# Performance work log

Hardware: AMD Instinct MI355X
Metric: run time of the kernel (lower is better)

The kernel has to match this reference:

```python
import jax, jax.numpy as jnp
import numpy as np
import math

B, L, D, H = 4, 1024, 768, 12   # docs, seq_len, hidden, attn heads
E, M, P = 24, 4, 552            # entities/doc, mentions/entity, pairs/doc
EMB, BLK, NL = 768, 64, 97      # emb_size, block_size, num relation labels


def setup_inputs() -> dict:
    key = jax.random.key(0)
    ks = jax.random.split(key, 12)
    s = 0.02  # weight init scale
    return {
        "sequence_output": jax.random.normal(ks[0], (B, L, D), jnp.float32),
        "attention": jax.random.uniform(ks[1], (B, H, L, L), jnp.float32),
        "W_q": jax.random.normal(ks[2], (D, D), jnp.float32) * s,
        "W_k": jax.random.normal(ks[3], (D, D), jnp.float32) * s,
        "head_W": jax.random.normal(ks[4], (2 * D, EMB), jnp.float32) * s,
        "head_b": jax.random.normal(ks[5], (EMB,), jnp.float32) * s,
        "tail_W": jax.random.normal(ks[6], (2 * D, EMB), jnp.float32) * s,
        "tail_b": jax.random.normal(ks[7], (EMB,), jnp.float32) * s,
        "bil_W": jax.random.normal(ks[8], (EMB * BLK, NL), jnp.float32) * s,
        "bil_b": jax.random.normal(ks[9], (NL,), jnp.float32) * s,
        "mention_pos": jax.random.randint(ks[10], (B, E, M), 0, L - 2),
        "hts": jax.random.randint(ks[11], (B, P, 2), 0, E),
    }


def reference(sequence_output, attention, W_q, W_k, head_W, head_b,
              tail_W, tail_b, bil_W, bil_b, mention_pos, hts):
    offset = 1  # bert-style [CLS] offset
    pos = mention_pos + offset                     # [B,E,M] token index of each mention
    bb = jnp.arange(B)[:, None, None]

    # --- mention gathers (padded version of the ragged python loops) ---
    # per-mention attention rows: attention[b, :, pos, :] -> [B,E,M,H,L]
    att_q = attention.transpose(0, 2, 1, 3)        # [B,L,H,L]
    ment_att = att_q[bb, pos]                      # [B,E,M,H,L]
    ent_att = ment_att.mean(axis=2)                # [B,E,H,L]  (mean over mentions)
    # mention embeddings (GAT stage = identity here): [B,E,M,D]
    ment_emb = sequence_output[bb, pos]

    # --- localized context rs via head*tail attention product ---
    bb2 = jnp.arange(B)[:, None]
    h_att = ent_att[bb2, hts[:, :, 0]]             # [B,P,H,L]
    t_att = ent_att[bb2, hts[:, :, 1]]             # [B,P,H,L]
    ht_att = (h_att * t_att).mean(axis=2)          # [B,P,L] (mean over heads)
    ht_att = ht_att / (ht_att.sum(axis=-1, keepdims=True) + 1e-5)
    rs = jnp.einsum('bld,bpl->bpd', sequence_output, ht_att)  # [B,P,D]

    R = B * P
    rs_f = rs.reshape(R, D)

    # --- entity representations via mention-level attention pooling ---
    h_ment = ment_emb[bb2, hts[:, :, 0]].reshape(R, M, D)
    t_ment = ment_emb[bb2, hts[:, :, 1]].reshape(R, M, D)
    q_c = rs_f @ W_q                               # [R,D]
    inv = 1.0 / math.sqrt(D)

    def pool(ment):
        k = ment.reshape(-1, D) @ W_k
        k = k.reshape(R, M, D)
        scores = jnp.einsum('rmd,rd->rm', k, q_c) * inv
        w = jax.nn.softmax(scores, axis=-1)
        return jnp.einsum('rm,rmd->rd', w, ment)

    h_ent = pool(h_ment)                           # [R,D]
    t_ent = pool(t_ment)                           # [R,D]

    # --- extractors + grouped bilinear classifier ---
    hs = jnp.tanh(jnp.concatenate([h_ent, rs_f], axis=1) @ head_W + head_b)
    ts = jnp.tanh(jnp.concatenate([t_ent, rs_f], axis=1) @ tail_W + tail_b)
    K = EMB // BLK
    b1 = hs.reshape(R, K, BLK)
    b2 = ts.reshape(R, K, BLK)
    bl = (b1[:, :, :, None] * b2[:, :, None, :]).reshape(R, EMB * BLK)
    logits = bl @ bil_W + bil_b                    # [R,NL]
    return logits
```

## Files before the change

### kernel.cpp

```cpp
#include <hip/hip_runtime.h>
#include <hip/hip_bf16.h>
#include <math.h>

#define Bc 4
#define Lc 1024
#define Dc 768
#define Hc 12
#define Ec 24
#define Mc 4
#define Pc 552
#define EMBc 768
#define NLc 97
#define Rc (Bc*Pc)
#define KSPL 48
#define HT_ABS (35*32*512)

typedef __attribute__((ext_vector_type(4))) float f32x4;
typedef __attribute__((ext_vector_type(8))) short short8;
typedef __attribute__((ext_vector_type(4))) unsigned short us4;
typedef _Float16 f16x8 __attribute__((ext_vector_type(8)));

static __device__ __forceinline__ unsigned short f2bf(float x){
  unsigned int u = __float_as_uint(x);
  unsigned int r = u + 0x7fffu + ((u >> 16) & 1u);
  return (unsigned short)(r >> 16);
}
static __device__ __forceinline__ unsigned short f2h(float x){
  _Float16 h = (_Float16)x;
  return __builtin_bit_cast(unsigned short, h);
}
static __device__ __forceinline__ float h2f(unsigned short x){
  return (float)__builtin_bit_cast(_Float16, x);
}
static __device__ __forceinline__ size_t flin_off(int r, int kk, int KT){
  return ((size_t)(r>>4)*KT + (kk>>5))*512 + (size_t)((((kk&31)>>3)*16 + (r&15))*8) + (kk&7);
}

__global__ __launch_bounds__(256) void k_prep(const float* __restrict__ bilW, unsigned short* __restrict__ Wbf,
                                              const float* __restrict__ seq, unsigned short* __restrict__ seqf,
                                              const float* __restrict__ W_q, unsigned short* __restrict__ Wq_f,
                                              const float* __restrict__ W_k, unsigned short* __restrict__ Wk_f,
                                              const float* __restrict__ headW, unsigned short* __restrict__ headW_f,
                                              const float* __restrict__ tailW, unsigned short* __restrict__ tailW_f,
                                              const float* __restrict__ att, const int* __restrict__ mpos,
                                              float* __restrict__ ent_att,
                                              unsigned short* __restrict__ ment_bf){
  int bx = blockIdx.x;
  int tid = threadIdx.x;
  __shared__ float t[64][65];
  if (bx < 1536){
    const float* Ws = bilW + (size_t)bx*32*NLc;
    unsigned short* o = Wbf + (size_t)bx*4480;
    float* w = &t[0][0];
    for (int idx = tid; idx < 32*NLc; idx += 256)
      w[idx] = Ws[idx];
    __syncthreads();
    #pragma unroll
    for (int q8 = 0; q8 < 18; q8++){
      int idx = q8*256 + tid;
      if (idx < 4480){
        int n = idx / 40, kk = idx - n*40;
        float v = (kk < 32 && n < NLc) ? w[kk*NLc + n] : 0.f;
        o[idx] = f2h(v);
      }
    }
    return;
  }
  if (bx >= 3168){
    int blk = bx - 3168;
    int h  = blk % Hc;
    int be = blk / Hc;
    int b  = be / Ec;
    int p0 = mpos[be*Mc+0]+1, p1 = mpos[be*Mc+1]+1;
    int p2 = mpos[be*Mc+2]+1, p3 = mpos[be*Mc+3]+1;
    const float* ab = att + ((size_t)b*Hc + h)*Lc*Lc;
    const float* a0 = ab + (size_t)p0*Lc;
    const float* a1 = ab + (size_t)p1*Lc;
    const float* a2 = ab + (size_t)p2*Lc;
    const float* a3 = ab + (size_t)p3*Lc;
    float* o = ent_att + (size_t)blk*Lc;
    int l4 = tid*4;
    float4 v0 = *(const float4*)(a0 + l4);
    float4 v1 = *(const float4*)(a1 + l4);
    float4 v2 = *(const float4*)(a2 + l4);
    float4 v3 = *(const float4*)(a3 + l4);
    float4 ov;
    ov.x = 0.25f*(v0.x+v1.x+v2.x+v3.x);
    ov.y = 0.25f*(v0.y+v1.y+v2.y+v3.y);
    ov.z = 0.25f*(v0.z+v1.z+v2.z+v3.z);
    ov.w = 0.25f*(v0.w+v1.w+v2.w+v3.w);
    *(float4*)(o + l4) = ov;
    int gidx = blk*256 + tid;
    int d = gidx % Dc;
    int bem = gidx / Dc;
    int bb = bem / (Ec*Mc);
    int pos = mpos[bem] + 1;
    float v = seq[((size_t)bb*Lc + pos)*Dc + d];
    ment_bf[flin_off(bem, d, 24)] = f2bf(v);
    return;
  }
  bx -= 1536;
  const float* src; unsigned short* dst; int tk, tn, KTW;
  if (bx < 768){
    int z = bx / 192, rem = bx % 192;
    src = seq + (size_t)z*Lc*Dc; dst = seqf + (size_t)z*(Dc/16)*(Lc/32)*512;
    tk = rem % 16; tn = rem / 16; KTW = 32;
  } else if (bx < 768+144){
    int rem = bx - 768;
    src = W_q; dst = Wq_f; tk = rem % 12; tn = rem / 12; KTW = 24;
  } else if (bx < 768+288){
    int rem = bx - (768+144);
    src = W_k; dst = Wk_f; tk = rem % 12; tn = rem / 12; KTW = 24;
  } else if (bx < 768+288+288){
    int rem = bx - (768+288);
    src = headW; dst = headW_f; tk = rem % 24; tn = rem / 24; KTW = 48;
  } else {
    int rem = bx - (768+288+288);
    src = tailW; dst = tailW_f; tk = rem % 24; tn = rem / 24; KTW = 48;
  }
  int r0 = tk*64, c0 = tn*64;
  #pragma unroll
  for (int q8 = 0; q8 < 16; q8++){
    int idx = q8*256 + tid;
    int rr = idx >> 6, cc = idx & 63;
    t[rr][cc] = src[(size_t)(r0+rr)*768 + c0+cc];
  }
  __syncthreads();
  #pragma unroll
  for (int q8 = 0; q8 < 16; q8++){
    int idx = q8*256 + tid;
    int li = idx & 511, sub = idx >> 9;
    int nt_l = sub >> 1, kt_l = sub & 1;
    int lane = li >> 3, e = li & 7;
    int kl = kt_l*32 + (lane>>4)*8 + e;
    int nl = nt_l*16 + (lane&15);
    dst[ ((size_t)(c0/16 + nt_l)*KTW + (r0/32 + kt_l))*512 + li ] = f2bf(t[kl][nl]);
  }
}

__global__ __launch_bounds__(256) void k_ht_att(const float* __restrict__ ent_att,
                                                const int* __restrict__ hts,
                                                unsigned short* __restrict__ htbf){
  int b = blockIdx.x & 3;
  int p = blockIdx.x >> 2;
  unsigned short* o = htbf + (size_t)b*HT_ABS;
  int l4 = threadIdx.x*4;
  if (p >= Pc){
    us4 z4 = {0,0,0,0};
    *(us4*)(o + flin_off(p, l4, 32)) = z4;
    return;
  }
  int r = b*Pc + p;
  int hi = hts[r*2+0], ti = hts[r*2+1];
  const float* eh = ent_att + (size_t)(b*Ec+hi)*Hc*Lc;
  const float* et = ent_att + (size_t)(b*Ec+ti)*Hc*Lc;
  __shared__ float raw[Lc];
  __shared__ float wsum[4];
  float4 s4 = {0.f,0.f,0.f,0.f};
  #pragma unroll
  for (int h = 0; h < Hc; h++){
    float4 e1 = *(const float4*)&eh[h*Lc + l4];
    float4 e2 = *(const float4*)&et[h*Lc + l4];
    s4.x = fmaf(e1.x,e2.x,s4.x); s4.y = fmaf(e1.y,e2.y,s4.y);
    s4.z = fmaf(e1.z,e2.z,s4.z); s4.w = fmaf(e1.w,e2.w,s4.w);
  }
  s4.x *= (1.0f/Hc); s4.y *= (1.0f/Hc); s4.z *= (1.0f/Hc); s4.w *= (1.0f/Hc);
  *(float4*)&raw[l4] = s4;
  float lsum = s4.x+s4.y+s4.z+s4.w;
  for (int off = 32; off; off >>= 1) lsum += __shfl_down(lsum, off);
  if ((threadIdx.x & 63) == 0) wsum[threadIdx.x>>6] = lsum;
  __syncthreads();
  float inv = 1.0f/(wsum[0]+wsum[1]+wsum[2]+wsum[3] + 1e-5f);
  float4 rv = *(const float4*)&raw[l4];
  us4 v4;
  v4[0] = f2bf(rv.x*inv); v4[1] = f2bf(rv.y*inv);
  v4[2] = f2bf(rv.z*inv); v4[3] = f2bf(rv.w*inv);
  *(us4*)(o + flin_off(p, l4, 32)) = v4;
}

struct FJob {
  const unsigned short* A1; const unsigned short* W; const float* bias; void* C;
  int M; int mtmax; int Wktw; int rowsPerBatch;
  size_t Abs; size_t Wbs;
};
struct FJobs {
  FJob j[6]; int xs[7]; int n;
};

template<int KT1, int CT, int NT, int KCH>
__global__ __launch_bounds__(256) void k_fgemmN(FJobs P){
  int tid = threadIdx.x;
  int jx = 0;
  for (int tjob = 1; tjob < P.n; tjob++)
    if ((int)blockIdx.x >= P.xs[tjob]) jx = tjob;
  FJob j = P.j[jx];
  int mbx = blockIdx.x - P.xs[jx];
  int z = blockIdx.z;
  int lane = tid & 63, wid = tid >> 6;
  int row16 = lane & 15, oct = lane >> 4;

  __shared__ __align__(16) unsigned short Wlds[NT*KCH*512];
  const unsigned short* wpan = j.W + (size_t)z*j.Wbs + (size_t)(blockIdx.y*NT)*j.Wktw*512;

  int rb = mbx*128 + wid*32;
  int mt0 = rb >> 4;       if (mt0 >= j.mtmax) mt0 = j.mtmax - 1;
  int mt1 = (rb >> 4) + 1; if (mt1 >= j.mtmax) mt1 = j.mtmax - 1;
  const unsigned short* ap0 = j.A1 + (size_t)z*j.Abs + (size_t)mt0*KT1*512 + lane*8;
  const unsigned short* ap1 = j.A1 + (size_t)z*j.Abs + (size_t)mt1*KT1*512 + lane*8;
  f32x4 acc[2][NT];
  #pragma unroll
  for (int m = 0; m < 2; m++)
    #pragma unroll
    for (int n = 0; n < NT; n++) acc[m][n] = (f32x4){0.f,0.f,0.f,0.f};

  #pragma unroll
  for (int kc = 0; kc < KT1/KCH; kc++){
    {
      constexpr int UNITS = NT*KCH*64;
      #pragma unroll
      for (int it = 0; it < UNITS/256; ++it){
        int u = it*256 + tid;
        int f = u >> 6;
        int n = f / KCH, kt = f - n*KCH;
        size_t so = (((size_t)(n*j.Wktw + kc*KCH + kt)) << 9) + (size_t)((u & 63) << 3);
        __builtin_amdgcn_global_load_lds(
            (const __attribute__((address_space(1))) unsigned int*)(wpan + so),
            (__attribute__((address_space(3))) unsigned int*)((char*)Wlds + (size_t)u*16),
            16, 0, 0);
      }
    }
    __syncthreads();
    #pragma unroll 4
    for (int k2 = 0; k2 < KCH; k2++){
      int kt = kc*KCH + k2;
      short8 a0 = *(const short8*)(ap0 + (size_t)kt*512);
      short8 a1 = *(const short8*)(ap1 + (size_t)kt*512);
      #pragma unroll
      for (int n = 0; n < NT; n++){
        short8 bv = *(const short8*)&Wlds[(n*KCH + k2)*512 + lane*8];
        acc[0][n] = __builtin_amdgcn_mfma_f32_16x16x32_bf16(a0, bv, acc[0][n], 0, 0, 0);
        acc[1][n] = __builtin_amdgcn_mfma_f32_16x16x32_bf16(a1, bv, acc[1][n], 0, 0, 0);
      }
    }
    if (kc + 1 < KT1/KCH) __syncthreads();
  }

  int colb = blockIdx.y*(NT*16);
  #pragma unroll
  for (int m = 0; m < 2; m++)
    #pragma unroll
    for (int n = 0; n < NT; n++)
      #pragma unroll
      for (int jj = 0; jj < 4; jj++){
        int r = rb + m*16 + oct*4 + jj;
        if (r < j.M){
          int col = colb + n*16 + row16;
          float v = acc[m][n][jj];
          if (CT == 0 && j.bias) v += j.bias[col];
          int rg = z*j.rowsPerBatch + r;
          if (CT == 2){
            ((unsigned short*)j.C)[flin_off(rg, col, 24)] = f2bf(v);
          } else if (CT == 3){
            ((unsigned short*)j.C)[(size_t)rg*768 + col] = f2h(v);
          } else {
            ((float*)j.C)[(size_t)rg*768 + col] = v;
          }
        }
      }
}

__global__ __launch_bounds__(256) void k_pool(const unsigned short* __restrict__ km16,
                                              const unsigned short* __restrict__ q16,
                                              const unsigned short* __restrict__ rsWh16,
                                              const unsigned short* __restrict__ rsWt16,
                                              const unsigned short* __restrict__ mWh16,
                                              const unsigned short* __restrict__ mWt16,
                                              const float* __restrict__ headb,
                                              const float* __restrict__ tailb,
                                              const int* __restrict__ hts,
                                              unsigned short* __restrict__ hs16,
                                              unsigned short* __restrict__ ts16){
  int wid = threadIdx.x >> 6, lane = threadIdx.x & 63;
  int r = blockIdx.x*4 + wid;
  int b = r / Pc;
  float q[12];
  const unsigned short* qp = q16 + (size_t)r*Dc + lane;
  #pragma unroll
  for (int u = 0; u < 12; u++) q[u] = h2f(qp[u*64]);
  const float invs = 0.03608439182435161f;
  #pragma unroll
  for (int side = 0; side < 2; side++){
    int e = hts[r*2+side];
    const unsigned short* kb = km16 + (size_t)(b*Ec+e)*Mc*Dc + lane;
    float part[Mc] = {0.f,0.f,0.f,0.f};
    #pragma unroll
    for (int m = 0; m < Mc; m++)
      #pragma unroll
      for (int u = 0; u < 12; u++)
        part[m] = fmaf(h2f(kb[m*Dc + u*64]), q[u], part[m]);
    #pragma unroll
    for (int m = 0; m < Mc; m++)
      #pragma unroll
      for (int off = 1; off < 64; off <<= 1)
        part[m] += __shfl_xor(part[m], off);
    float mx = fmaxf(fmaxf(part[0],part[1]), fmaxf(part[2],part[3])) * invs;
    float w0 = expf(part[0]*invs - mx), w1 = expf(part[1]*invs - mx);
    float w2 = expf(part[2]*invs - mx), w3 = expf(part[3]*invs - mx);
    float isum = 1.0f/(w0+w1+w2+w3);
    w0 *= isum; w1 *= isum; w2 *= isum; w3 *= isum;
    const unsigned short* mW  = (side ? mWt16  : mWh16) + (size_t)(b*Ec+e)*Mc*Dc;
    const unsigned short* rsW = (side ? rsWt16 : rsWh16) + (size_t)r*Dc;
    const float* bias = side ? tailb : headb;
    unsigned short* o = (side ? ts16 : hs16) + (size_t)r*Dc;
    #pragma unroll
    for (int u = 0; u < 12; u++){
      int d = lane + u*64;
      float v = h2f(rsW[d]) + bias[d]
              + w0*h2f(mW[d]) + w1*h2f(mW[Dc+d]) + w2*h2f(mW[2*Dc+d]) + w3*h2f(mW[3*Dc+d]);
      o[d] = f2h(tanhf(v));
    }
  }
}

__global__ __launch_bounds__(256) void k_bilinear_mfma(
    const unsigned short* __restrict__ hs16, const unsigned short* __restrict__ ts16,
    const unsigned short* __restrict__ Wbf,
    unsigned short* __restrict__ partial)
{
  int mb = blockIdx.x / KSPL;
  int kb = blockIdx.x % KSPL;
  int k  = kb >> 2;
  int i0 = (kb & 3) * 16;

  int tid  = threadIdx.x;
  int lane = tid & 63;
  int wid  = tid >> 6;
  int row16 = lane & 15;
  int oct   = lane >> 4;

  int rbase = mb*256 + wid*64;

  __shared__ __align__(16) unsigned short Wlds[2][8960];

  f16x8 tsh[4][2];
  f16x8 hsh[4][2];
  #pragma unroll
  for (int m = 0; m < 4; m++){
    int r = rbase + m*16 + row16; if (r > Rc-1) r = Rc-1;
    const unsigned short* tp = ts16 + (size_t)r*EMBc + k*64;
    tsh[m][0] = __builtin_bit_cast(f16x8, *(const short8*)(tp + oct*8));
    tsh[m][1] = __builtin_bit_cast(f16x8, *(const short8*)(tp + 32 + oct*8));
    const unsigned short* hp = hs16 + (size_t)r*EMBc + k*64 + i0;
    hsh[m][0] = __builtin_bit_cast(f16x8, *(const short8*)(hp));
    hsh[m][1] = __builtin_bit_cast(f16x8, *(const short8*)(hp + 8));
  }

  const char* wsrc = (const char*)(Wbf + ((size_t)(k*128 + i0*2))*4480);

  #pragma unroll
  for (int rr = 0; rr < 5; rr++){
    int u = tid + rr*256;
    if (u < 1120)
      __builtin_amdgcn_global_load_lds(
        (const __attribute__((address_space(1))) unsigned int*)(wsrc + (size_t)u*16),
        (__attribute__((address_space(3))) unsigned int*)((char*)&Wlds[0][0] + u*16),
        16, 0, 0);
  }

  f32x4 acc[4][7];
  #pragma unroll
  for (int m = 0; m < 4; m++)
    #pragma unroll
    for (int n = 0; n < 7; n++) acc[m][n] = (f32x4){0.f,0.f,0.f,0.f};

  __syncthreads();

  #pragma unroll
  for (int cp = 0; cp < 16; cp++){
    int cur = cp & 1;
    if (cp < 15){
      const char* nsrc = wsrc + (size_t)(cp+1)*17920;
      #pragma unroll
      for (int rr = 0; rr < 5; rr++){
        int u = tid + rr*256;
        if (u < 1120)
          __builtin_amdgcn_global_load_lds(
            (const __attribute__((address_space(1))) unsigned int*)(nsrc + (size_t)u*16),
            (__attribute__((address_space(3))) unsigned int*)((char*)&Wlds[cur^1][0] + u*16),
            16, 0, 0);
      }
    }
    #pragma unroll
    for (int half = 0; half < 2; half++){
      f16x8 af[4];
      #pragma unroll
      for (int m = 0; m < 4; m++){
        _Float16 hv = hsh[m][cp>>3][cp&7];
        f16x8 hvb = {hv,hv,hv,hv,hv,hv,hv,hv};
        af[m] = tsh[m][half] * hvb;
      }
      #pragma unroll
      for (int n = 0; n < 7; n++){
        f16x8 bfr = __builtin_bit_cast(f16x8,
            *(const short8*)&Wlds[cur][half*4480 + (n*16 + row16)*40 + oct*8]);
        #pragma unroll
        for (int m = 0; m < 4; m++)
          acc[m][n] = __builtin_amdgcn_mfma_f32_16x16x32_f16(af[m], bfr, acc[m][n], 0, 0, 0);
      }
    }
    __syncthreads();
  }

  unsigned short* pk = partial + (size_t)kb*Rc*NLc;
  #pragma unroll
  for (int m = 0; m < 4; m++){
    #pragma unroll
    for (int n = 0; n < 7; n++){
      #pragma unroll
      for (int j = 0; j < 4; j++){
        int r = rbase + m*16 + oct*4 + j;
        int col = n*16 + row16;
        if (r < Rc && col < NLc)
          pk[(size_t)r*NLc + col] = f2h(acc[m][n][j]);
      }
    }
  }
}

__global__ __launch_bounds__(256) void k_reduce(const unsigned short* __restrict__ partial,
                                                const float* __restrict__ bilb,
                                                float* __restrict__ out){
  int idx = blockIdx.x*256 + threadIdx.x;
  if (idx >= Rc*NLc) return;
  int n = idx % NLc;
  float s = bilb[n];
  #pragma unroll
  for (int ks = 0; ks < KSPL; ks++) s += h2f(partial[(size_t)ks*Rc*NLc + idx]);
  out[idx] = s;
}

extern "C" void kernel_launch(void* const* d_in, const int* in_sizes, int n_in,
                              void* d_out, int out_size, void* d_ws, size_t ws_size,
                              hipStream_t stream){
  const float* seq   = (const float*)d_in[0];
  const float* att   = (const float*)d_in[1];
  const float* W_q   = (const float*)d_in[2];
  const float* W_k   = (const float*)d_in[3];
  const float* headW = (const float*)d_in[4];
  const float* headb = (const float*)d_in[5];
  const float* tailW = (const float*)d_in[6];
  const float* tailb = (const float*)d_in[7];
  const float* bilW  = (const float*)d_in[8];
  const float* bilb  = (const float*)d_in[9];
  const int*   mpos  = (const int*)d_in[10];
  const int*   hts   = (const int*)d_in[11];
  float* out = (float*)d_out;

  float* ws = (float*)d_ws;
  float* ent_att = ws;
  unsigned short* base = (unsigned short*)(ws + 1179648);
  unsigned short* q16     = base;
  unsigned short* km16    = q16 + 1695744;
  unsigned short* seqf    = km16 + 294912;
  unsigned short* htbf    = seqf + 3145728;
  unsigned short* rs_bf   = htbf + 4*HT_ABS;
  unsigned short* ment_bf = rs_bf + 1695744;
  unsigned short* Wq_f    = ment_bf + 294912;
  unsigned short* Wk_f    = Wq_f + 589824;
  unsigned short* headW_f = Wk_f + 589824;
  unsigned short* tailW_f = headW_f + 1179648;
  unsigned short* hs16    = tailW_f + 1179648;
  unsigned short* ts16    = hs16 + 1695744;
  unsigned short* Wbf     = ts16 + 1695744;
  unsigned short* rsWh16  = Wbf + 6881280;
  unsigned short* rsWt16  = rsWh16 + 1695744;
  unsigned short* mWh16   = rsWt16 + 1695744;
  unsigned short* mWt16   = mWh16 + 294912;
  unsigned short* partial = (unsigned short*)ws;

  k_prep   <<<4320, 256, 0, stream>>>(bilW, Wbf, seq, seqf, W_q, Wq_f, W_k, Wk_f,
                                      headW, headW_f, tailW, tailW_f,
                                      att, mpos, ent_att, ment_bf);
  k_ht_att <<<4*560, 256, 0, stream>>>(ent_att, hts, htbf);
  {
    FJobs P{};
    P.j[0] = { htbf, seqf, nullptr, rs_bf, Pc, 35, 32, Pc,
               (size_t)HT_ABS, (size_t)(48*32*512) };
    P.xs[0] = 0; P.xs[1] = 5; P.n = 1;
    k_fgemmN<32,2,2,32><<<dim3(5,24,4), 256, 0, stream>>>(P);
  }
  {
    FJobs P{};
    P.j[0] = { rs_bf,   Wq_f,              nullptr, q16,    Rc,  138, 24, 0, 0, 0 };
    P.j[1] = { ment_bf, Wk_f,              nullptr, km16,   384,  24, 24, 0, 0, 0 };
    P.j[2] = { rs_bf,   headW_f + 24*512,  nullptr, rsWh16, Rc,  138, 48, 0, 0, 0 };
    P.j[3] = { rs_bf,   tailW_f + 24*512,  nullptr, rsWt16, Rc,  138, 48, 0, 0, 0 };
    P.j[4] = { ment_bf, headW_f,           nullptr, mWh16,  384,  24, 48, 0, 0, 0 };
    P.j[5] = { ment_bf, tailW_f,           nullptr, mWt16,  384,  24, 48, 0, 0, 0 };
    P.xs[0]=0; P.xs[1]=18; P.xs[2]=21; P.xs[3]=39; P.xs[4]=57; P.xs[5]=60; P.xs[6]=63;
    P.n = 6;
    k_fgemmN<24,3,4,12><<<dim3(63,12), 256, 0, stream>>>(P);
  }
  k_pool   <<<Rc/4, 256, 0, stream>>>(km16, q16, rsWh16, rsWt16, mWh16, mWt16,
                                      headb, tailb, hts, hs16, ts16);
  k_bilinear_mfma<<<9*KSPL, 256, 0, stream>>>(hs16, ts16, Wbf, partial);
  k_reduce <<<(Rc*NLc+255)/256, 256, 0, stream>>>(partial, bilb, out);
}
```

Before: 122.3 us.

## Fuse three GEMMs sharing an A operand into one kernel reusing A loads

```diff
diff --git a/kernel.cpp b/kernel.cpp
--- a/kernel.cpp
+++ b/kernel.cpp
@@ -183,18 +183,11 @@
   int M; int mtmax; int Wktw; int rowsPerBatch;
   size_t Abs; size_t Wbs;
 };
-struct FJobs {
-  FJob j[6]; int xs[7]; int n;
-};
 
 template<int KT1, int CT, int NT, int KCH>
-__global__ __launch_bounds__(256) void k_fgemmN(FJobs P){
+__global__ __launch_bounds__(256) void k_fgemmN(FJob j){
   int tid = threadIdx.x;
-  int jx = 0;
-  for (int tjob = 1; tjob < P.n; tjob++)
-    if ((int)blockIdx.x >= P.xs[tjob]) jx = tjob;
-  FJob j = P.j[jx];
-  int mbx = blockIdx.x - P.xs[jx];
+  int mbx = blockIdx.x;
   int z = blockIdx.z;
   int lane = tid & 63, wid = tid >> 6;
   int row16 = lane & 15, oct = lane >> 4;
@@ -255,18 +248,97 @@
         int r = rb + m*16 + oct*4 + jj;
         if (r < j.M){
           int col = colb + n*16 + row16;
-          float v = acc[m][n][jj];
-          if (CT == 0 && j.bias) v += j.bias[col];
           int rg = z*j.rowsPerBatch + r;
-          if (CT == 2){
-            ((unsigned short*)j.C)[flin_off(rg, col, 24)] = f2bf(v);
-          } else if (CT == 3){
-            ((unsigned short*)j.C)[(size_t)rg*768 + col] = f2h(v);
-          } else {
-            ((float*)j.C)[(size_t)rg*768 + col] = v;
+          ((unsigned short*)j.C)[flin_off(rg, col, 24)] = f2bf(acc[m][n][jj]);
+        }
+      }
+}
+
+struct F3 {
+  const unsigned short* A1;
+  const unsigned short* W0; const unsigned short* W1; const unsigned short* W2;
+  unsigned short* C0; unsigned short* C1; unsigned short* C2;
+  int M; int mtmax; int ktw0; int ktw1; int ktw2;
+};
+
+template<int KT1, int NT, int KCH>
+__global__ __launch_bounds__(256) void k_fgemm3(F3 j0, F3 j1, int nx0){
+  int tid = threadIdx.x;
+  F3 j = ((int)blockIdx.x < nx0) ? j0 : j1;
+  int mbx = ((int)blockIdx.x < nx0) ? blockIdx.x : blockIdx.x - nx0;
+  int lane = tid & 63, wid = tid >> 6;
+  int row16 = lane & 15, oct = lane >> 4;
+  const unsigned short* Ws[3] = { j.W0, j.W1, j.W2 };
+  unsigned short* Cs[3] = { j.C0, j.C1, j.C2 };
+  const int ktws[3] = { j.ktw0, j.ktw1, j.ktw2 };
+
+  __shared__ __align__(16) unsigned short Wlds[3][NT*KCH*512];
+
+  int rb = mbx*128 + wid*32;
+  int mt0 = rb >> 4;  if (mt0 >= j.mtmax) mt0 = j.mtmax - 1;
+  int mt1 = mt0 + 1;  if (mt1 >= j.mtmax) mt1 = j.mtmax - 1;
+  const unsigned short* ap0 = j.A1 + (size_t)mt0*KT1*512 + lane*8;
+  const unsigned short* ap1 = j.A1 + (size_t)mt1*KT1*512 + lane*8;
+
+  f32x4 acc[3][2][NT];
+  #pragma unroll
+  for (int s = 0; s < 3; s++)
+    #pragma unroll
+    for (int m = 0; m < 2; m++)
+      #pragma unroll
+      for (int n = 0; n < NT; n++) acc[s][m][n] = (f32x4){0.f,0.f,0.f,0.f};
+
+  #pragma unroll
+  for (int kc = 0; kc < KT1/KCH; kc++){
+    #pragma unroll
+    for (int s = 0; s < 3; s++){
+      const unsigned short* wpan = Ws[s] + (size_t)(blockIdx.y*NT)*ktws[s]*512;
+      constexpr int UNITS = NT*KCH*64;
+      #pragma unroll
+      for (int it = 0; it < UNITS/256; ++it){
+        int u = it*256 + tid;
+        int f = u >> 6;
+        int n = f / KCH, kt = f - n*KCH;
+        size_t so = (((size_t)(n*ktws[s] + kc*KCH + kt)) << 9) + (size_t)((u & 63) << 3);
+        __builtin_amdgcn_global_load_lds(
+            (const __attribute__((address_space(1))) unsigned int*)(wpan + so),
+            (__attribute__((address_space(3))) unsigned int*)((char*)&Wlds[s][0] + (size_t)u*16),
+            16, 0, 0);
+      }
+    }
+    __syncthreads();
+    #pragma unroll 2
+    for (int k2 = 0; k2 < KCH; k2++){
+      int kt = kc*KCH + k2;
+      short8 a0 = *(const short8*)(ap0 + (size_t)kt*512);
+      short8 a1 = *(const short8*)(ap1 + (size_t)kt*512);
+      #pragma unroll
+      for (int s = 0; s < 3; s++)
+        #pragma unroll
+        for (int n = 0; n < NT; n++){
+          short8 bv = *(const short8*)&Wlds[s][(n*KCH + k2)*512 + lane*8];
+          acc[s][0][n] = __builtin_amdgcn_mfma_f32_16x16x32_bf16(a0, bv, acc[s][0][n], 0, 0, 0);
+          acc[s][1][n] = __builtin_amdgcn_mfma_f32_16x16x32_bf16(a1, bv, acc[s][1][n], 0, 0, 0);
+        }
+    }
+    if (kc + 1 < KT1/KCH) __syncthreads();
+  }
+
+  int colb = blockIdx.y*(NT*16);
+  #pragma unroll
+  for (int s = 0; s < 3; s++)
+    #pragma unroll
+    for (int m = 0; m < 2; m++)
+      #pragma unroll
+      for (int n = 0; n < NT; n++)
+        #pragma unroll
+        for (int jj = 0; jj < 4; jj++){
+          int r = rb + m*16 + oct*4 + jj;
+          if (r < j.M){
+            int col = colb + n*16 + row16;
+            Cs[s][(size_t)r*768 + col] = f2h(acc[s][m][n][jj]);
           }
         }
-      }
 }
 
 __global__ __launch_bounds__(256) void k_pool(const unsigned short* __restrict__ km16,
@@ -483,23 +555,16 @@
                                       att, mpos, ent_att, ment_bf);
   k_ht_att <<<4*560, 256, 0, stream>>>(ent_att, hts, htbf);
   {
-    FJobs P{};
-    P.j[0] = { htbf, seqf, nullptr, rs_bf, Pc, 35, 32, Pc,
-               (size_t)HT_ABS, (size_t)(48*32*512) };
-    P.xs[0] = 0; P.xs[1] = 5; P.n = 1;
-    k_fgemmN<32,2,2,32><<<dim3(5,24,4), 256, 0, stream>>>(P);
+    FJob jrs = { htbf, seqf, nullptr, rs_bf, Pc, 35, 32, Pc,
+                 (size_t)HT_ABS, (size_t)(48*32*512) };
+    k_fgemmN<32,2,2,32><<<dim3(5,24,4), 256, 0, stream>>>(jrs);
   }
   {
-    FJobs P{};
-    P.j[0] = { rs_bf,   Wq_f,              nullptr, q16,    Rc,  138, 24, 0, 0, 0 };
-    P.j[1] = { ment_bf, Wk_f,              nullptr, km16,   384,  24, 24, 0, 0, 0 };
-    P.j[2] = { rs_bf,   headW_f + 24*512,  nullptr, rsWh16, Rc,  138, 48, 0, 0, 0 };
-    P.j[3] = { rs_bf,   tailW_f + 24*512,  nullptr, rsWt16, Rc,  138, 48, 0, 0, 0 };
-    P.j[4] = { ment_bf, headW_f,           nullptr, mWh16,  384,  24, 48, 0, 0, 0 };
-    P.j[5] = { ment_bf, tailW_f,           nullptr, mWt16,  384,  24, 48, 0, 0, 0 };
-    P.xs[0]=0; P.xs[1]=18; P.xs[2]=21; P.xs[3]=39; P.xs[4]=57; P.xs[5]=60; P.xs[6]=63;
-    P.n = 6;
-    k_fgemmN<24,3,4,12><<<dim3(63,12), 256, 0, stream>>>(P);
+    F3 jA = { rs_bf,   Wq_f, headW_f + 24*512, tailW_f + 24*512,
+              q16,  rsWh16, rsWt16, Rc,  138, 24, 48, 48 };
+    F3 jB = { ment_bf, Wk_f, headW_f,          tailW_f,
+              km16, mWh16,  mWt16,  384, 24,  24, 48, 48 };
+    k_fgemm3<24,2,12><<<dim3(21,24), 256, 0, stream>>>(jA, jB, 18);
   }
   k_pool   <<<Rc/4, 256, 0, stream>>>(km16, q16, rsWh16, rsWt16, mWh16, mWt16,
                                       headb, tailb, hts, hs16, ts16);
```

Result: no change. 122.2 us, median of 2 (-0.1%).
